# Performance work log

Hardware: AMD Instinct MI355X
Metric: run time of the kernel (lower is better)

The kernel has to match this reference:

```python
import jax, jax.numpy as jnp
import numpy as np

DIM = 256
HEADS = 8
HEAD_DIM = DIM // HEADS            # 32
EXP_HEADS = 16                     # int(2.0 * HEADS)
N = 2048
E = 32768
SCALE = HEAD_DIM ** -0.5
MASK_VALUE = -1e9  # safe stand-in for -finfo.max (avoids inf after the head-expand linear)


def setup_inputs() -> dict:
    key = jax.random.key(0)
    ks = jax.random.split(key, 9)
    s = 0.05
    return {
        "x": jax.random.normal(ks[0], (N, DIM), dtype=jnp.float32),
        "edges": jax.random.normal(ks[1], (N, DIM), dtype=jnp.float32),
        "edge_index": jax.random.randint(ks[2], (2, E), 0, N, dtype=jnp.int64),
        "Wq": jax.random.normal(ks[3], (DIM, DIM), dtype=jnp.float32) * s,
        "Wk": jax.random.normal(ks[4], (DIM, DIM), dtype=jnp.float32) * s,
        "Wv": jax.random.normal(ks[5], (EXP_HEADS * HEAD_DIM, DIM), dtype=jnp.float32) * s,
        "Wev": jax.random.normal(ks[6], (EXP_HEADS * HEAD_DIM, DIM), dtype=jnp.float32) * s,
        "Wexp": jax.random.normal(ks[7], (EXP_HEADS, HEADS), dtype=jnp.float32) * s,
        "Wout": jax.random.normal(ks[8], (DIM, EXP_HEADS * HEAD_DIM), dtype=jnp.float32) * s,
    }


def reference(x, edges, edge_index, Wq, Wk, Wv, Wev, Wexp, Wout):
    n = x.shape[0]
    # projections; torch Linear weight is (out, in) -> x @ W.T
    q = (x @ Wq.T).reshape(n, HEADS, HEAD_DIM).transpose(1, 0, 2)            # h n d
    k = (x @ Wk.T).reshape(n, HEADS, HEAD_DIM).transpose(1, 0, 2) * SCALE    # h n d
    v = (x @ Wv.T).reshape(n, EXP_HEADS, HEAD_DIM).transpose(1, 0, 2)        # e n d
    edge_v = (edges @ Wev.T).reshape(n, EXP_HEADS, HEAD_DIM).transpose(1, 0, 2)

    src, dst = edge_index[0], edge_index[1]
    # per-edge elementwise dot product: gather q at src, k at dst
    ew = jnp.einsum('hpd,hpd->hp', q[:, src], k[:, dst])                     # h E

    # scatter into dense (heads, n, n) attention, masked elsewhere
    attn = jnp.full((HEADS, n, n), MASK_VALUE, dtype=x.dtype)
    attn = attn.at[:, src, dst].set(ew)

    # head-expand linear over the head axis: (n m h) @ (exp h)^T -> exp n m
    attn = jnp.einsum('hnm,eh->enm', attn, Wexp)
    attn = jax.nn.softmax(attn, axis=-1)

    # graph Laplacian: I - A
    attn = jnp.eye(n, dtype=x.dtype)[None, :, :] - attn                      # e n m

    vv = v + edge_v                                                          # e n d
    out = jnp.einsum('enm,emd->end', attn, vv)                               # e n d
    out = out.transpose(1, 0, 2).reshape(n, EXP_HEADS * HEAD_DIM)
    out = out @ Wout.T                                                       # n dim
    return out
```

## Files before the change

### kernel.cpp

```cpp
#include <hip/hip_runtime.h>

#define NN 2048
#define DIMM 256
#define HEADS 8
#define HEAD_DIM 32
#define EXPH 16
#define E_EDGES 32768
#define VDIM 512
#define PW 1024
#define SCALE_F 0.17677669529663687f
#define MASKV -1.0e9f
#define SLOTW 64

typedef __attribute__((ext_vector_type(8))) short short8;
typedef __attribute__((ext_vector_type(4))) float f32x4;

__device__ __forceinline__ unsigned short f2bf(float f) {
    unsigned int u = __float_as_uint(f);
    unsigned int r = (u + 0x7FFFu + ((u >> 16) & 1u)) >> 16;
    return (unsigned short)r;
}
__device__ __forceinline__ float bflo(unsigned int u) { return __uint_as_float(u << 16); }
__device__ __forceinline__ float bfhi(unsigned int u) { return __uint_as_float(u & 0xFFFF0000u); }

__device__ __forceinline__ int load_edge(const int* __restrict__ ei32, int is64, int idx) {
    return is64 ? ei32[2 * idx] : ei32[idx];
}

__global__ __launch_bounds__(256) void convert_init_kernel(
    const float* __restrict__ x, const float* __restrict__ edges,
    const float* __restrict__ Wq, const float* __restrict__ Wk,
    const float* __restrict__ Wv, const float* __restrict__ Wev,
    const float* __restrict__ Wout,
    unsigned short* __restrict__ xb, unsigned short* __restrict__ eb,
    unsigned short* __restrict__ Wqb, unsigned short* __restrict__ Wkb,
    unsigned short* __restrict__ Wvb, unsigned short* __restrict__ Wevb,
    unsigned short* __restrict__ Woutb,
    float* __restrict__ partialX, float* __restrict__ partialE,
    int* __restrict__ slotCnt)
{
    __shared__ float lds[4][260];
    int b = blockIdx.x;
    int t = threadIdx.x;
    if (b >= 1536) {
        slotCnt[(b - 1536) * 256 + t] = 0;
        return;
    }
    int idx = b * 256 + t;
    const float* src; unsigned short* dst; int loc;
    if      (idx < 131072) { src = x;     dst = xb;    loc = idx; }
    else if (idx < 262144) { src = edges; dst = eb;    loc = idx - 131072; }
    else if (idx < 278528) { src = Wq;    dst = Wqb;   loc = idx - 262144; }
    else if (idx < 294912) { src = Wk;    dst = Wkb;   loc = idx - 278528; }
    else if (idx < 327680) { src = Wv;    dst = Wvb;   loc = idx - 294912; }
    else if (idx < 360448) { src = Wev;   dst = Wevb;  loc = idx - 327680; }
    else                   { src = Wout;  dst = Woutb; loc = idx - 360448; }
    float4 v = *(const float4*)(src + (size_t)loc * 4);
    ushort4 o;
    o.x = f2bf(v.x); o.y = f2bf(v.y); o.z = f2bf(v.z); o.w = f2bf(v.w);
    *(ushort4*)(dst + (size_t)loc * 4) = o;
    if (b < 1024) {
        int lr = t >> 6;
        int lc = (t & 63) * 4;
        lds[lr][lc + 0] = v.x; lds[lr][lc + 1] = v.y;
        lds[lr][lc + 2] = v.z; lds[lr][lc + 3] = v.w;
        __syncthreads();
        float s = lds[0][t] + lds[1][t] + lds[2][t] + lds[3][t];
        if (b < 512) partialX[(size_t)b * 256 + t] = s;
        else         partialE[(size_t)(b - 512) * 256 + t] = s;
    }
}

__global__ __launch_bounds__(256) void proj_aux_kernel(
    const unsigned short* __restrict__ xb, const unsigned short* __restrict__ eb,
    const unsigned short* __restrict__ Wqb, const unsigned short* __restrict__ Wkb,
    const unsigned short* __restrict__ Wvb, const unsigned short* __restrict__ Wevb,
    unsigned short* __restrict__ Pb,
    const int* __restrict__ ei32, int* __restrict__ slotCnt, unsigned int* __restrict__ slots,
    const float* __restrict__ partialX, const float* __restrict__ partialE,
    const float* __restrict__ Wv32, const float* __restrict__ Wev32,
    float* __restrict__ colsum)
{
    __shared__ float xsumS[256], esumS[256], partS[8][36];
    int t = threadIdx.x;
    int jb = blockIdx.y;

    if (jb == 16) {
        int bx = blockIdx.x;
        int nz = __syncthreads_count(ei32[2 * t + 1] != 0);
        int is64 = (nz == 0);
        #pragma unroll
        for (int r = 0; r < 2; r++) {
            int p = bx * 512 + r * 256 + t;
            int s = load_edge(ei32, is64, p);
            int d = load_edge(ei32, is64, E_EDGES + p);
            int pos = atomicAdd(&slotCnt[s], 1);
            if (pos < SLOTW)
                slots[(size_t)s * SLOTW + pos] = (unsigned int)(p * 2048 + d);
        }
        float accx[8] = {0.f,0.f,0.f,0.f,0.f,0.f,0.f,0.f};
        float acce[8] = {0.f,0.f,0.f,0.f,0.f,0.f,0.f,0.f};
        for (int r = 0; r < 512; r += 8) {
            #pragma unroll
            for (int j = 0; j < 8; j++) {
                accx[j] += partialX[(size_t)(r + j) * 256 + t];
                acce[j] += partialE[(size_t)(r + j) * 256 + t];
            }
        }
        xsumS[t] = ((accx[0] + accx[1]) + (accx[2] + accx[3]))
                 + ((accx[4] + accx[5]) + (accx[6] + accx[7]));
        esumS[t] = ((acce[0] + acce[1]) + (acce[2] + acce[3]))
                 + ((acce[4] + acce[5]) + (acce[6] + acce[7]));
        __syncthreads();
        int cl = t >> 5;
        int c  = bx * 8 + cl;
        int k0 = (t & 31) * 8;
        const float* wv = Wv32  + (size_t)c * 256 + k0;
        const float* we = Wev32 + (size_t)c * 256 + k0;
        float s = 0.f;
        #pragma unroll
        for (int j = 0; j < 8; j++)
            s += xsumS[k0 + j] * wv[j] + esumS[k0 + j] * we[j];
        partS[cl][t & 31] = s;
        __syncthreads();
        if (t < 8) {
            float acc = 0.f;
            for (int g = 0; g < 32; g++) acc += partS[t][g];
            colsum[bx * 8 + t] = acc;
        }
        return;
    }

    int lane = t & 63;
    int wave = t >> 6;
    int wm = wave >> 1;
    int wn = wave & 1;
    int rowT = blockIdx.x * 32;
    int colT = jb * 64;

    const unsigned short* Wb; int wbase; int nseg = 1;
    if (jb < 4)      { Wb = Wqb; wbase = jb * 64; }
    else if (jb < 8) { Wb = Wkb; wbase = (jb - 4) * 64; }
    else             { Wb = Wvb; wbase = (jb - 8) * 64; nseg = 2; }

    int arow = rowT + wm * 16 + (lane & 15);
    int koff = (lane >> 4) * 8;

    f32x4 acc0 = {0.f, 0.f, 0.f, 0.f};
    f32x4 acc1 = {0.f, 0.f, 0.f, 0.f};

    for (int seg = 0; seg < nseg; ++seg) {
        const unsigned short* Ab = (seg == 0) ? xb : eb;
        const unsigned short* Wm = (seg == 0) ? Wb : Wevb;
        const unsigned short* ap  = Ab + (size_t)arow * DIMM + koff;
        const unsigned short* b0p = Wm + (size_t)(wbase + wn * 32 + (lane & 15)) * DIMM + koff;
        const unsigned short* b1p = b0p + 16 * DIMM;
        #pragma unroll
        for (int ks = 0; ks < 8; ks++) {
            short8 af = *(const short8*)(ap  + ks * 32);
            short8 b0 = *(const short8*)(b0p + ks * 32);
            short8 b1 = *(const short8*)(b1p + ks * 32);
            acc0 = __builtin_amdgcn_mfma_f32_16x16x32_bf16(af, b0, acc0, 0, 0, 0);
            acc1 = __builtin_amdgcn_mfma_f32_16x16x32_bf16(af, b1, acc1, 0, 0, 0);
        }
    }
    float sc = (jb >= 4 && jb < 8) ? SCALE_F : 1.0f;
    int crow0 = rowT + wm * 16 + (lane >> 4) * 4;
    int ccol  = colT + wn * 32 + (lane & 15);
    #pragma unroll
    for (int r = 0; r < 4; r++) {
        Pb[(size_t)(crow0 + r) * PW + ccol]      = f2bf(acc0[r] * sc);
        Pb[(size_t)(crow0 + r) * PW + ccol + 16] = f2bf(acc1[r] * sc);
    }
}

__global__ __launch_bounds__(256) void laplacian_kernel(
    const int* __restrict__ slotCnt, const unsigned int* __restrict__ slots,
    const float* __restrict__ Wexp, const float* __restrict__ colsum,
    const unsigned short* __restrict__ Pb, unsigned short* __restrict__ out2b)
{
    __shared__ unsigned int pkS[SLOTW], srtS[SLOTW];
    __shared__ int liveS[SLOTW];
    __shared__ float ewS[SLOTW][HEADS];
    __shared__ float aS[SLOTW][EXPH];
    __shared__ float WexpS[EXPH * HEADS];
    __shared__ float qS[DIMM];
    __shared__ float maxP[4][EXPH], sumP[4][EXPH];
    __shared__ float wmaskS[EXPH], invDS[EXPH];
    __shared__ int Dcnt;
    int n = blockIdx.x;
    int t = threadIdx.x;
    int cnt = slotCnt[n];
    if (cnt > SLOTW) cnt = SLOTW;
    if (t == 0) Dcnt = 0;
    if (t < EXPH * HEADS) WexpS[t] = Wexp[t];
    if (t < cnt) pkS[t] = slots[(size_t)n * SLOTW + t];
    if (t < 128) {
        unsigned int u = ((const unsigned int*)(Pb + (size_t)n * PW))[t];
        qS[2 * t]     = bflo(u);
        qS[2 * t + 1] = bfhi(u);
    }
    __syncthreads();
    if (t < cnt) {
        unsigned int pk = pkS[t];
        int rank = 0;
        #pragma unroll 4
        for (int j = 0; j < cnt; j++) rank += (pkS[j] < pk) ? 1 : 0;
        srtS[rank] = pk;
    }
    __syncthreads();
    if (t < cnt) {
        unsigned int d = srtS[t] & 2047u;
        int live = 1;
        #pragma unroll 4
        for (int j = t + 1; j < cnt; j++)
            live &= ((srtS[j] & 2047u) != d) ? 1 : 0;
        liveS[t] = live;
        if (live) atomicAdd(&Dcnt, 1);
    }
    {
        int h = t & 7;
        const float* qh = qS + h * 32;
        for (int i = t >> 3; i < cnt; i += 32) {
            int dsti = (int)(srtS[i] & 2047u);
            const uint4* kr = (const uint4*)(Pb + (size_t)dsti * PW + 256 + h * 32);
            float s = 0.f;
            #pragma unroll
            for (int m = 0; m < 4; m++) {
                uint4 u = kr[m];
                const float* qq = qh + m * 8;
                s += qq[0] * bflo(u.x) + qq[1] * bfhi(u.x)
                   + qq[2] * bflo(u.y) + qq[3] * bfhi(u.y)
                   + qq[4] * bflo(u.z) + qq[5] * bfhi(u.z)
                   + qq[6] * bflo(u.w) + qq[7] * bfhi(u.w);
            }
            ewS[i][h] = s;
        }
    }
    __syncthreads();
    int e = t & 15;
    float Me = 0.f;
    #pragma unroll
    for (int h = 0; h < HEADS; h++) Me += MASKV * WexpS[e * HEADS + h];
    float m = -3.0e38f;
    for (int idx = t; idx < cnt * EXPH; idx += 256) {
        int i = idx >> 4;
        float a = 0.f;
        #pragma unroll
        for (int hh = 0; hh < HEADS; hh++) a += ewS[i][hh] * WexpS[e * HEADS + hh];
        aS[i][e] = a;
        if (liveS[i] && a > m) m = a;
    }
    m = fmaxf(m, __shfl_xor(m, 16));
    m = fmaxf(m, __shfl_xor(m, 32));
    if ((t & 0x30) == 0) maxP[t >> 6][e] = m;
    __syncthreads();
    float rmax = fmaxf(fmaxf(maxP[0][e], maxP[1][e]), fmaxf(maxP[2][e], maxP[3][e]));
    rmax = fmaxf(rmax, Me);
    float ds = 0.f;
    for (int idx = t; idx < cnt * EXPH; idx += 256) {
        int i = idx >> 4;
        float w = liveS[i] ? expf(aS[i][e] - rmax) : 0.f;
        aS[i][e] = w;
        ds += w;
    }
    ds += __shfl_xor(ds, 16);
    ds += __shfl_xor(ds, 32);
    if ((t & 0x30) == 0) sumP[t >> 6][e] = ds;
    __syncthreads();
    if (t < EXPH) {
        float wmE = expf(Me - rmax);
        float denom = ((sumP[0][t] + sumP[1][t]) + (sumP[2][t] + sumP[3][t]))
                    + (float)(NN - Dcnt) * wmE;
        wmaskS[t] = wmE / denom;
        invDS[t]  = 1.0f / denom;
    }
    __syncthreads();
    int e2 = t >> 4;
    float wm = wmaskS[e2];
    float invD = invDS[e2];
    unsigned int uv = ((const unsigned int*)(Pb + (size_t)n * PW + 512))[t];
    float2 cv = ((const float2*)colsum)[t];
    float ax = bflo(uv) - wm * cv.x;
    float ay = bfhi(uv) - wm * cv.y;
    int i = 0;
    for (; i + 8 <= cnt; i += 8) {
        unsigned int u[8];
        float w[8];
        #pragma unroll
        for (int j = 0; j < 8; j++)
            u[j] = ((const unsigned int*)(Pb + (size_t)(srtS[i + j] & 2047u) * PW + 512))[t];
        #pragma unroll
        for (int j = 0; j < 8; j++)
            w[j] = liveS[i + j] ? (wm - aS[i + j][e2] * invD) : 0.f;
        #pragma unroll
        for (int j = 0; j < 8; j++) { ax += w[j] * bflo(u[j]); ay += w[j] * bfhi(u[j]); }
    }
    for (; i < cnt; i++) {
        unsigned int ub = ((const unsigned int*)(Pb + (size_t)(srtS[i] & 2047u) * PW + 512))[t];
        float w = liveS[i] ? (wm - aS[i][e2] * invD) : 0.f;
        ax += w * bflo(ub); ay += w * bfhi(ub);
    }
    unsigned int* o = (unsigned int*)(out2b + (size_t)n * VDIM);
    o[t] = (unsigned int)f2bf(ax) | ((unsigned int)f2bf(ay) << 16);
}

__global__ __launch_bounds__(256) void outgemm_mfma_kernel(
    const unsigned short* __restrict__ Ab, const unsigned short* __restrict__ Wb,
    float* __restrict__ C)
{
    int t = threadIdx.x;
    int lane = t & 63;
    int wn = t >> 6;
    int rowT = blockIdx.x * 16;
    int colT = blockIdx.y * 64 + wn * 16;

    int arow = rowT + (lane & 15);
    int koff = (lane >> 4) * 8;

    f32x4 accA = {0.f, 0.f, 0.f, 0.f};
    f32x4 accB = {0.f, 0.f, 0.f, 0.f};

    const unsigned short* ap = Ab + (size_t)arow * VDIM + koff;
    const unsigned short* bp = Wb + (size_t)(colT + (lane & 15)) * VDIM + koff;
    #pragma unroll
    for (int ks = 0; ks < 8; ks++) {
        short8 afA = *(const short8*)(ap + ks * 32);
        short8 bfA = *(const short8*)(bp + ks * 32);
        accA = __builtin_amdgcn_mfma_f32_16x16x32_bf16(afA, bfA, accA, 0, 0, 0);
        short8 afB = *(const short8*)(ap + (ks + 8) * 32);
        short8 bfB = *(const short8*)(bp + (ks + 8) * 32);
        accB = __builtin_amdgcn_mfma_f32_16x16x32_bf16(afB, bfB, accB, 0, 0, 0);
    }
    int crow0 = rowT + (lane >> 4) * 4;
    int ccol  = colT + (lane & 15);
    #pragma unroll
    for (int r = 0; r < 4; r++)
        C[(size_t)(crow0 + r) * DIMM + ccol] = accA[r] + accB[r];
}

extern "C" void kernel_launch(void* const* d_in, const int* in_sizes, int n_in,
                              void* d_out, int out_size, void* d_ws, size_t ws_size,
                              hipStream_t stream) {
    const float* x     = (const float*)d_in[0];
    const float* edges = (const float*)d_in[1];
    const int*   ei32  = (const int*)d_in[2];
    const float* Wq    = (const float*)d_in[3];
    const float* Wk    = (const float*)d_in[4];
    const float* Wv    = (const float*)d_in[5];
    const float* Wev   = (const float*)d_in[6];
    const float* Wexp  = (const float*)d_in[7];
    const float* Wout  = (const float*)d_in[8];
    float* out = (float*)d_out;

    char* ws = (char*)d_ws;
    size_t off = 0;
    auto alloc = [&](size_t bytes) -> void* {
        void* p = ws + off;
        off = (off + bytes + 255) & ~(size_t)255;
        return p;
    };
    unsigned short* Pb    = (unsigned short*)alloc((size_t)NN * PW * 2);
    float* partialX       = (float*)alloc((size_t)512 * 256 * 4);
    float* partialE       = (float*)alloc((size_t)512 * 256 * 4);
    float* colsum         = (float*)alloc(VDIM * 4);
    unsigned short* xb    = (unsigned short*)alloc((size_t)NN * DIMM * 2);
    unsigned short* eb    = (unsigned short*)alloc((size_t)NN * DIMM * 2);
    unsigned short* Wqb   = (unsigned short*)alloc((size_t)DIMM * DIMM * 2);
    unsigned short* Wkb   = (unsigned short*)alloc((size_t)DIMM * DIMM * 2);
    unsigned short* Wvb   = (unsigned short*)alloc((size_t)VDIM * DIMM * 2);
    unsigned short* Wevb  = (unsigned short*)alloc((size_t)VDIM * DIMM * 2);
    unsigned short* Woutb = (unsigned short*)alloc((size_t)DIMM * VDIM * 2);
    unsigned short* out2b = (unsigned short*)alloc((size_t)NN * VDIM * 2);
    int* slotCnt          = (int*)alloc(NN * 4);
    unsigned int* slots   = (unsigned int*)alloc((size_t)NN * SLOTW * 4);
    (void)ws_size; (void)in_sizes; (void)n_in; (void)out_size;

    convert_init_kernel<<<1544, 256, 0, stream>>>(x, edges, Wq, Wk, Wv, Wev, Wout,
                                                  xb, eb, Wqb, Wkb, Wvb, Wevb, Woutb,
                                                  partialX, partialE, slotCnt);
    proj_aux_kernel<<<dim3(64, 17), 256, 0, stream>>>(xb, eb, Wqb, Wkb, Wvb, Wevb, Pb,
                                                      ei32, slotCnt, slots,
                                                      partialX, partialE, Wv, Wev, colsum);
    laplacian_kernel<<<NN, 256, 0, stream>>>(slotCnt, slots, Wexp, colsum, Pb, out2b);
    outgemm_mfma_kernel<<<dim3(128, 4), 256, 0, stream>>>(out2b, Woutb, out);
}
```

Before: 63.85 us.

## Split column-sum reduction and edge scatter into separate parallel kernel before projection

Moves the partial-sum reduction and edge bucketing out of the 64 auxiliary blocks of the projection kernel into a new 576-block kernel. There each column is reduced by its own block with a tree reduction. The projection kernel now runs 1024 blocks, and its first 512 also compute one colsum entry each via a 256-wide dot product. The goal is to remove the long serial tail in the 64 aux blocks, which each looped over 512 partial rows. The cost is an extra kernel launch and a dependency barrier between the reduction and the projection.

```diff
diff --git a/kernel.cpp b/kernel.cpp
--- a/kernel.cpp
+++ b/kernel.cpp
@@ -71,22 +71,30 @@
     }
 }
 
-__global__ __launch_bounds__(256) void proj_aux_kernel(
-    const unsigned short* __restrict__ xb, const unsigned short* __restrict__ eb,
-    const unsigned short* __restrict__ Wqb, const unsigned short* __restrict__ Wkb,
-    const unsigned short* __restrict__ Wvb, const unsigned short* __restrict__ Wevb,
-    unsigned short* __restrict__ Pb,
-    const int* __restrict__ ei32, int* __restrict__ slotCnt, unsigned int* __restrict__ slots,
+__global__ __launch_bounds__(256) void red_scatter_kernel(
     const float* __restrict__ partialX, const float* __restrict__ partialE,
-    const float* __restrict__ Wv32, const float* __restrict__ Wev32,
-    float* __restrict__ colsum)
-{
-    __shared__ float xsumS[256], esumS[256], partS[8][36];
-    int t = threadIdx.x;
-    int jb = blockIdx.y;
-
-    if (jb == 16) {
-        int bx = blockIdx.x;
+    float* __restrict__ xsumG, float* __restrict__ esumG,
+    const int* __restrict__ ei32, int* __restrict__ slotCnt,
+    unsigned int* __restrict__ slots)
+{
+    __shared__ float tree[256];
+    int blk = blockIdx.x;
+    int t = threadIdx.x;
+    if (blk < 512) {
+        const float* part = (blk < 256) ? partialX : partialE;
+        int c = blk & 255;
+        tree[t] = part[(size_t)t * 256 + c] + part[(size_t)(t + 256) * 256 + c];
+        __syncthreads();
+        for (int w = 128; w > 0; w >>= 1) {
+            if (t < w) tree[t] += tree[t + w];
+            __syncthreads();
+        }
+        if (t == 0) {
+            if (blk < 256) xsumG[c] = tree[0];
+            else           esumG[c] = tree[0];
+        }
+    } else {
+        int bx = blk - 512;
         int nz = __syncthreads_count(ei32[2 * t + 1] != 0);
         int is64 = (nz == 0);
         #pragma unroll
@@ -98,79 +106,78 @@
             if (pos < SLOTW)
                 slots[(size_t)s * SLOTW + pos] = (unsigned int)(p * 2048 + d);
         }
-        float accx[8] = {0.f,0.f,0.f,0.f,0.f,0.f,0.f,0.f};
-        float acce[8] = {0.f,0.f,0.f,0.f,0.f,0.f,0.f,0.f};
-        for (int r = 0; r < 512; r += 8) {
+    }
+}
+
+__global__ __launch_bounds__(256) void proj_gemv_kernel(
+    const unsigned short* __restrict__ xb, const unsigned short* __restrict__ eb,
+    const unsigned short* __restrict__ Wqb, const unsigned short* __restrict__ Wkb,
+    const unsigned short* __restrict__ Wvb, const unsigned short* __restrict__ Wevb,
+    unsigned short* __restrict__ Pb,
+    const float* __restrict__ xsumG, const float* __restrict__ esumG,
+    const float* __restrict__ Wv32, const float* __restrict__ Wev32,
+    float* __restrict__ colsum)
+{
+    __shared__ float tree[256];
+    int blk = blockIdx.x;
+    int t = threadIdx.x;
+    int bx = blk & 63;
+    int jb = blk >> 6;
+
+    {
+        int lane = t & 63;
+        int wave = t >> 6;
+        int wm = wave >> 1;
+        int wn = wave & 1;
+        int rowT = bx * 32;
+        int colT = jb * 64;
+
+        const unsigned short* Wb; int wbase; int nseg = 1;
+        if (jb < 4)      { Wb = Wqb; wbase = jb * 64; }
+        else if (jb < 8) { Wb = Wkb; wbase = (jb - 4) * 64; }
+        else             { Wb = Wvb; wbase = (jb - 8) * 64; nseg = 2; }
+
+        int arow = rowT + wm * 16 + (lane & 15);
+        int koff = (lane >> 4) * 8;
+
+        f32x4 acc0 = {0.f, 0.f, 0.f, 0.f};
+        f32x4 acc1 = {0.f, 0.f, 0.f, 0.f};
+
+        for (int seg = 0; seg < nseg; ++seg) {
+            const unsigned short* Ab = (seg == 0) ? xb : eb;
+            const unsigned short* Wm = (seg == 0) ? Wb : Wevb;
+            const unsigned short* ap  = Ab + (size_t)arow * DIMM + koff;
+            const unsigned short* b0p = Wm + (size_t)(wbase + wn * 32 + (lane & 15)) * DIMM + koff;
+            const unsigned short* b1p = b0p + 16 * DIMM;
             #pragma unroll
-            for (int j = 0; j < 8; j++) {
-                accx[j] += partialX[(size_t)(r + j) * 256 + t];
-                acce[j] += partialE[(size_t)(r + j) * 256 + t];
+            for (int ks = 0; ks < 8; ks++) {
+                short8 af = *(const short8*)(ap  + ks * 32);
+                short8 b0 = *(const short8*)(b0p + ks * 32);
+                short8 b1 = *(const short8*)(b1p + ks * 32);
+                acc0 = __builtin_amdgcn_mfma_f32_16x16x32_bf16(af, b0, acc0, 0, 0, 0);
+                acc1 = __builtin_amdgcn_mfma_f32_16x16x32_bf16(af, b1, acc1, 0, 0, 0);
             }
         }
-        xsumS[t] = ((accx[0] + accx[1]) + (accx[2] + accx[3]))
-                 + ((accx[4] + accx[5]) + (accx[6] + accx[7]));
-        esumS[t] = ((acce[0] + acce[1]) + (acce[2] + acce[3]))
-                 + ((acce[4] + acce[5]) + (acce[6] + acce[7]));
+        float sc = (jb >= 4 && jb < 8) ? SCALE_F : 1.0f;
+        int crow0 = rowT + wm * 16 + (lane >> 4) * 4;
+        int ccol  = colT + wn * 32 + (lane & 15);
+        #pragma unroll
+        for (int r = 0; r < 4; r++) {
+            Pb[(size_t)(crow0 + r) * PW + ccol]      = f2bf(acc0[r] * sc);
+            Pb[(size_t)(crow0 + r) * PW + ccol + 16] = f2bf(acc1[r] * sc);
+        }
+    }
+    if (blk < 512) {
+        int c = blk;
+        float v = xsumG[t] * Wv32[(size_t)c * 256 + t]
+                + esumG[t] * Wev32[(size_t)c * 256 + t];
+        tree[t] = v;
         __syncthreads();
-        int cl = t >> 5;
-        int c  = bx * 8 + cl;
-        int k0 = (t & 31) * 8;
-        const float* wv = Wv32  + (size_t)c * 256 + k0;
-        const float* we = Wev32 + (size_t)c * 256 + k0;
-        float s = 0.f;
-        #pragma unroll
-        for (int j = 0; j < 8; j++)
-            s += xsumS[k0 + j] * wv[j] + esumS[k0 + j] * we[j];
-        partS[cl][t & 31] = s;
-        __syncthreads();
-        if (t < 8) {
-            float acc = 0.f;
-            for (int g = 0; g < 32; g++) acc += partS[t][g];
-            colsum[bx * 8 + t] = acc;
-        }
-        return;
-    }
-
-    int lane = t & 63;
-    int wave = t >> 6;
-    int wm = wave >> 1;
-    int wn = wave & 1;
-    int rowT = blockIdx.x * 32;
-    int colT = jb * 64;
-
-    const unsigned short* Wb; int wbase; int nseg = 1;
-    if (jb < 4)      { Wb = Wqb; wbase = jb * 64; }
-    else if (jb < 8) { Wb = Wkb; wbase = (jb - 4) * 64; }
-    else             { Wb = Wvb; wbase = (jb - 8) * 64; nseg = 2; }
-
-    int arow = rowT + wm * 16 + (lane & 15);
-    int koff = (lane >> 4) * 8;
-
-    f32x4 acc0 = {0.f, 0.f, 0.f, 0.f};
-    f32x4 acc1 = {0.f, 0.f, 0.f, 0.f};
-
-    for (int seg = 0; seg < nseg; ++seg) {
-        const unsigned short* Ab = (seg == 0) ? xb : eb;
-        const unsigned short* Wm = (seg == 0) ? Wb : Wevb;
-        const unsigned short* ap  = Ab + (size_t)arow * DIMM + koff;
-        const unsigned short* b0p = Wm + (size_t)(wbase + wn * 32 + (lane & 15)) * DIMM + koff;
-        const unsigned short* b1p = b0p + 16 * DIMM;
-        #pragma unroll
-        for (int ks = 0; ks < 8; ks++) {
-            short8 af = *(const short8*)(ap  + ks * 32);
-            short8 b0 = *(const short8*)(b0p + ks * 32);
-            short8 b1 = *(const short8*)(b1p + ks * 32);
-            acc0 = __builtin_amdgcn_mfma_f32_16x16x32_bf16(af, b0, acc0, 0, 0, 0);
-            acc1 = __builtin_amdgcn_mfma_f32_16x16x32_bf16(af, b1, acc1, 0, 0, 0);
-        }
-    }
-    float sc = (jb >= 4 && jb < 8) ? SCALE_F : 1.0f;
-    int crow0 = rowT + wm * 16 + (lane >> 4) * 4;
-    int ccol  = colT + wn * 32 + (lane & 15);
-    #pragma unroll
-    for (int r = 0; r < 4; r++) {
-        Pb[(size_t)(crow0 + r) * PW + ccol]      = f2bf(acc0[r] * sc);
-        Pb[(size_t)(crow0 + r) * PW + ccol + 16] = f2bf(acc1[r] * sc);
+        for (int w = 128; w > 0; w >>= 1) {
+            if (t < w) tree[t] += tree[t + w];
+            __syncthreads();
+        }
+        if (t == 0) colsum[c] = tree[0];
     }
 }
 
@@ -363,6 +370,8 @@
     unsigned short* Pb    = (unsigned short*)alloc((size_t)NN * PW * 2);
     float* partialX       = (float*)alloc((size_t)512 * 256 * 4);
     float* partialE       = (float*)alloc((size_t)512 * 256 * 4);
+    float* xsumG          = (float*)alloc(256 * 4);
+    float* esumG          = (float*)alloc(256 * 4);
     float* colsum         = (float*)alloc(VDIM * 4);
     unsigned short* xb    = (unsigned short*)alloc((size_t)NN * DIMM * 2);
     unsigned short* eb    = (unsigned short*)alloc((size_t)NN * DIMM * 2);
@@ -379,9 +388,10 @@
     convert_init_kernel<<<1544, 256, 0, stream>>>(x, edges, Wq, Wk, Wv, Wev, Wout,
                                                   xb, eb, Wqb, Wkb, Wvb, Wevb, Woutb,
                                                   partialX, partialE, slotCnt);
-    proj_aux_kernel<<<dim3(64, 17), 256, 0, stream>>>(xb, eb, Wqb, Wkb, Wvb, Wevb, Pb,
-                                                      ei32, slotCnt, slots,
-                                                      partialX, partialE, Wv, Wev, colsum);
+    red_scatter_kernel<<<576, 256, 0, stream>>>(partialX, partialE, xsumG, esumG,
+                                                ei32, slotCnt, slots);
+    proj_gemv_kernel<<<1024, 256, 0, stream>>>(xb, eb, Wqb, Wkb, Wvb, Wevb, Pb,
+                                               xsumG, esumG, Wv, Wev, colsum);
     laplacian_kernel<<<NN, 256, 0, stream>>>(slotCnt, slots, Wexp, colsum, Pb, out2b);
     outgemm_mfma_kernel<<<dim3(128, 4), 256, 0, stream>>>(out2b, Woutb, out);
 }
```

New measurement: 57.76 us (median of 2 runs). 1.11x faster.
